# Kernel tuning notes

Measured on AMD Instinct MI355X. Metric: run time of the kernel, lower is better.

## Reference

```python
import jax, jax.numpy as jnp
import numpy as np

OUT_FEATURES = 4096
IN_FEATURES = 4096
GROUP_SIZE = 128


def setup_inputs() -> dict:
    key = jax.random.key(0)
    k1, k2, k3, k4, k5 = jax.random.split(key, 5)
    x = jax.random.normal(k1, (4, 2048, IN_FEATURES), dtype=jnp.float32)
    # two 4-bit codes per byte-like int32 element
    packed = jax.random.randint(k2, (OUT_FEATURES * IN_FEATURES // 2,), 0, 256, dtype=jnp.int32)
    n_groups = OUT_FEATURES * IN_FEATURES // GROUP_SIZE
    scales = jax.random.uniform(k3, (n_groups,), dtype=jnp.float32) * 0.02 + 1e-3
    offsets = jax.random.normal(k4, (n_groups,), dtype=jnp.float32) * 0.01
    bias = jax.random.normal(k5, (OUT_FEATURES,), dtype=jnp.float32)
    return {"x": x, "packed": packed, "scales": scales, "offsets": offsets, "bias": bias}


def _dequant(packed, scales, offsets):
    # unpack low/high nibbles -> int codes in [0, 15]
    low = packed & 0xF
    high = (packed >> 4) & 0xF
    codes = jnp.stack([low, high], axis=-1).reshape(-1).astype(jnp.float32)  # [out*in]
    # per-group affine dequant: w = code * scale + offset
    w = codes.reshape(-1, GROUP_SIZE) * scales[:, None] + offsets[:, None]
    return w.reshape(OUT_FEATURES, IN_FEATURES)


def reference(x, packed, scales, offsets, bias):
    weight = _dequant(packed, scales, offsets)  # [out, in]
    # F.linear: x @ W^T + b
    return jnp.einsum('bsi,oi->bso', x, weight) + bias
```

## Files before the change

kernel.cpp:

```cpp
#include <hip/hip_runtime.h>
#include <hip/hip_bf16.h>
#include <stdint.h>

#define IN_F   4096
#define OUT_F  4096
#define M_TOT  8192

typedef __bf16 bf16x8 __attribute__((ext_vector_type(8)));
typedef float  floatx4 __attribute__((ext_vector_type(4)));

__device__ __forceinline__ unsigned f2bf_bits(float f) {
    union { float f; uint32_t u; } v; v.f = f;
    uint32_t r = v.u + 0x7FFF + ((v.u >> 16) & 1);
    return r >> 16;
}

__device__ __forceinline__ void gl_lds16(const void* g, void* l) {
    __builtin_amdgcn_global_load_lds(
        (const __attribute__((address_space(1))) void*)g,
        (__attribute__((address_space(3))) void*)l, 16, 0, 0);
}

#define X_BLOCKS 16384
#define W_BLOCKS 8192

__global__ void prep_kernel(const float* __restrict__ x, ushort* __restrict__ xb,
                            const int* __restrict__ packed,
                            const float* __restrict__ scales,
                            const float* __restrict__ offsets,
                            ushort* __restrict__ wb) {
    if (blockIdx.x < X_BLOCKS) {
        int i = blockIdx.x * 256 + threadIdx.x;
        float4 v0 = reinterpret_cast<const float4*>(x)[2 * i];
        float4 v1 = reinterpret_cast<const float4*>(x)[2 * i + 1];
        uint4 o;
        o.x = f2bf_bits(v0.x) | (f2bf_bits(v0.y) << 16);
        o.y = f2bf_bits(v0.z) | (f2bf_bits(v0.w) << 16);
        o.z = f2bf_bits(v1.x) | (f2bf_bits(v1.y) << 16);
        o.w = f2bf_bits(v1.z) | (f2bf_bits(v1.w) << 16);
        reinterpret_cast<uint4*>(xb)[i] = o;
    } else {
        int i = (blockIdx.x - X_BLOCKS) * 256 + threadIdx.x;
        int4 p = reinterpret_cast<const int4*>(packed)[i];
        int g = i >> 4;
        float s = scales[g], off = offsets[g];
        uint4 ov;
        ov.x = f2bf_bits((float)(p.x & 0xF) * s + off) |
               (f2bf_bits((float)((p.x >> 4) & 0xF) * s + off) << 16);
        ov.y = f2bf_bits((float)(p.y & 0xF) * s + off) |
               (f2bf_bits((float)((p.y >> 4) & 0xF) * s + off) << 16);
        ov.z = f2bf_bits((float)(p.z & 0xF) * s + off) |
               (f2bf_bits((float)((p.z >> 4) & 0xF) * s + off) << 16);
        ov.w = f2bf_bits((float)(p.w & 0xF) * s + off) |
               (f2bf_bits((float)((p.w >> 4) & 0xF) * s + off) << 16);
        reinterpret_cast<uint4*>(wb)[i] = ov;
    }
}

__global__ void gemm_kernel(const ushort* __restrict__ A,
                            const ushort* __restrict__ B,
                            const float* __restrict__ bias,
                            float* __restrict__ C) {
    __shared__ __align__(16) ushort As[128 * 32];
    __shared__ __align__(16) ushort Bs[128 * 32];

    const int tid  = threadIdx.x;
    const int wave = tid >> 6;
    const int lane = tid & 63;
    const int quad = lane >> 4;
    const int l16  = lane & 15;
    const int wm   = wave >> 1;
    const int wn   = wave & 1;

    const int bm = blockIdx.y;
    const int bn = blockIdx.x;

    const int c0 = tid, c1 = 256 + tid;
    const int r0 = c0 >> 2, l0 = (c0 & 3) ^ ((r0 >> 1) & 3);
    const int r1 = c1 >> 2, l1 = (c1 & 3) ^ ((r1 >> 1) & 3);

    const ushort* gA0 = A + (size_t)(bm * 128 + r0) * IN_F + l0 * 8;
    const ushort* gA1 = A + (size_t)(bm * 128 + r1) * IN_F + l1 * 8;
    const ushort* gB0 = B + (size_t)(bn * 128 + r0) * IN_F + l0 * 8;
    const ushort* gB1 = B + (size_t)(bn * 128 + r1) * IN_F + l1 * 8;

    char* lA0 = (char*)As + wave * 1024;
    char* lA1 = (char*)As + 4096 + wave * 1024;
    char* lB0 = (char*)Bs + wave * 1024;
    char* lB1 = (char*)Bs + 4096 + wave * 1024;

    floatx4 acc[4][4] = {};

    const int arow = wm * 64 + l16;
    const int brow = wn * 64 + l16;
    const int koff = (quad ^ ((l16 >> 1) & 3)) * 8;

    for (int k0 = 0; k0 < IN_F; k0 += 32) {
        gl_lds16(gA0, lA0);
        gl_lds16(gA1, lA1);
        gl_lds16(gB0, lB0);
        gl_lds16(gB1, lB1);
        gA0 += 32; gA1 += 32; gB0 += 32; gB1 += 32;
        __syncthreads();

        bf16x8 af[4], bfr[4];
#pragma unroll
        for (int mi = 0; mi < 4; ++mi)
            af[mi] = *reinterpret_cast<const bf16x8*>(&As[(arow + mi * 16) * 32 + koff]);
#pragma unroll
        for (int ni = 0; ni < 4; ++ni)
            bfr[ni] = *reinterpret_cast<const bf16x8*>(&Bs[(brow + ni * 16) * 32 + koff]);

#pragma unroll
        for (int mi = 0; mi < 4; ++mi)
#pragma unroll
            for (int ni = 0; ni < 4; ++ni)
                acc[mi][ni] = __builtin_amdgcn_mfma_f32_16x16x32_bf16(
                    af[mi], bfr[ni], acc[mi][ni], 0, 0, 0);

        __syncthreads();
    }

    const float* biasp = bias + bn * 128 + wn * 64 + l16;
    float* Cp = C + (size_t)(bm * 128 + wm * 64 + quad * 4) * OUT_F + bn * 128 + wn * 64 + l16;
#pragma unroll
    for (int mi = 0; mi < 4; ++mi) {
#pragma unroll
        for (int ni = 0; ni < 4; ++ni) {
            float bv = biasp[ni * 16];
#pragma unroll
            for (int r = 0; r < 4; ++r)
                Cp[(size_t)(mi * 16 + r) * OUT_F + ni * 16] = acc[mi][ni][r] + bv;
        }
    }
}

extern "C" void kernel_launch(void* const* d_in, const int* in_sizes, int n_in,
                              void* d_out, int out_size, void* d_ws, size_t ws_size,
                              hipStream_t stream) {
    const float* x       = (const float*)d_in[0];
    const int*   packed  = (const int*)d_in[1];
    const float* scales  = (const float*)d_in[2];
    const float* offsets = (const float*)d_in[3];
    const float* bias    = (const float*)d_in[4];
    float* out = (float*)d_out;

    ushort* xb = (ushort*)d_ws;
    ushort* wb = (ushort*)((char*)d_ws + (size_t)M_TOT * IN_F * 2);

    prep_kernel<<<X_BLOCKS + W_BLOCKS, 256, 0, stream>>>(x, xb, packed, scales, offsets, wb);

    dim3 grid(OUT_F / 128, M_TOT / 128);
    gemm_kernel<<<grid, 256, 0, stream>>>(xb, wb, bias, out);
}
```

Before: 549.4 us.

## Fuse fp32-to-bf16 activation conversion into GEMM tile loads

Drops the separate pass that converted the activations to bf16 in workspace. The GEMM now streams fp32 activation tiles straight into LDS with a new XOR swizzle and converts them to bf16 in registers before the MFMA. This removes a full read and write of the activation tensor, but doubles the A-tile global traffic and LDS footprint per k-step and repeats the conversion once for each of the 32 column blocks.

```diff
diff --git a/kernel.cpp b/kernel.cpp
--- a/kernel.cpp
+++ b/kernel.cpp
@@ -21,47 +21,31 @@
         (__attribute__((address_space(3))) void*)l, 16, 0, 0);
 }
 
-#define X_BLOCKS 16384
-#define W_BLOCKS 8192
-
-__global__ void prep_kernel(const float* __restrict__ x, ushort* __restrict__ xb,
-                            const int* __restrict__ packed,
-                            const float* __restrict__ scales,
-                            const float* __restrict__ offsets,
-                            ushort* __restrict__ wb) {
-    if (blockIdx.x < X_BLOCKS) {
-        int i = blockIdx.x * 256 + threadIdx.x;
-        float4 v0 = reinterpret_cast<const float4*>(x)[2 * i];
-        float4 v1 = reinterpret_cast<const float4*>(x)[2 * i + 1];
-        uint4 o;
-        o.x = f2bf_bits(v0.x) | (f2bf_bits(v0.y) << 16);
-        o.y = f2bf_bits(v0.z) | (f2bf_bits(v0.w) << 16);
-        o.z = f2bf_bits(v1.x) | (f2bf_bits(v1.y) << 16);
-        o.w = f2bf_bits(v1.z) | (f2bf_bits(v1.w) << 16);
-        reinterpret_cast<uint4*>(xb)[i] = o;
-    } else {
-        int i = (blockIdx.x - X_BLOCKS) * 256 + threadIdx.x;
-        int4 p = reinterpret_cast<const int4*>(packed)[i];
-        int g = i >> 4;
-        float s = scales[g], off = offsets[g];
-        uint4 ov;
-        ov.x = f2bf_bits((float)(p.x & 0xF) * s + off) |
-               (f2bf_bits((float)((p.x >> 4) & 0xF) * s + off) << 16);
-        ov.y = f2bf_bits((float)(p.y & 0xF) * s + off) |
-               (f2bf_bits((float)((p.y >> 4) & 0xF) * s + off) << 16);
-        ov.z = f2bf_bits((float)(p.z & 0xF) * s + off) |
-               (f2bf_bits((float)((p.z >> 4) & 0xF) * s + off) << 16);
-        ov.w = f2bf_bits((float)(p.w & 0xF) * s + off) |
-               (f2bf_bits((float)((p.w >> 4) & 0xF) * s + off) << 16);
-        reinterpret_cast<uint4*>(wb)[i] = ov;
-    }
+__global__ void dequant_kernel(const int* __restrict__ packed,
+                               const float* __restrict__ scales,
+                               const float* __restrict__ offsets,
+                               ushort* __restrict__ wb) {
+    int i = blockIdx.x * 256 + threadIdx.x;
+    int4 p = reinterpret_cast<const int4*>(packed)[i];
+    int g = i >> 4;
+    float s = scales[g], off = offsets[g];
+    uint4 ov;
+    ov.x = f2bf_bits((float)(p.x & 0xF) * s + off) |
+           (f2bf_bits((float)((p.x >> 4) & 0xF) * s + off) << 16);
+    ov.y = f2bf_bits((float)(p.y & 0xF) * s + off) |
+           (f2bf_bits((float)((p.y >> 4) & 0xF) * s + off) << 16);
+    ov.z = f2bf_bits((float)(p.z & 0xF) * s + off) |
+           (f2bf_bits((float)((p.z >> 4) & 0xF) * s + off) << 16);
+    ov.w = f2bf_bits((float)(p.w & 0xF) * s + off) |
+           (f2bf_bits((float)((p.w >> 4) & 0xF) * s + off) << 16);
+    reinterpret_cast<uint4*>(wb)[i] = ov;
 }
 
-__global__ void gemm_kernel(const ushort* __restrict__ A,
+__global__ void gemm_kernel(const float* __restrict__ A,
                             const ushort* __restrict__ B,
                             const float* __restrict__ bias,
                             float* __restrict__ C) {
-    __shared__ __align__(16) ushort As[128 * 32];
+    __shared__ __align__(16) float  Asf[128 * 32];
     __shared__ __align__(16) ushort Bs[128 * 32];
 
     const int tid  = threadIdx.x;
@@ -75,38 +59,55 @@
     const int bm = blockIdx.y;
     const int bn = blockIdx.x;
 
-    const int c0 = tid, c1 = 256 + tid;
-    const int r0 = c0 >> 2, l0 = (c0 & 3) ^ ((r0 >> 1) & 3);
-    const int r1 = c1 >> 2, l1 = (c1 & 3) ^ ((r1 >> 1) & 3);
+    const int ar = tid >> 3;
+    const int al = (tid & 7) ^ (ar & 7);
+    const float* gA0 = A + (size_t)(bm * 128 +  0 + ar) * IN_F + al * 4;
+    const float* gA1 = A + (size_t)(bm * 128 + 32 + ar) * IN_F + al * 4;
+    const float* gA2 = A + (size_t)(bm * 128 + 64 + ar) * IN_F + al * 4;
+    const float* gA3 = A + (size_t)(bm * 128 + 96 + ar) * IN_F + al * 4;
 
-    const ushort* gA0 = A + (size_t)(bm * 128 + r0) * IN_F + l0 * 8;
-    const ushort* gA1 = A + (size_t)(bm * 128 + r1) * IN_F + l1 * 8;
-    const ushort* gB0 = B + (size_t)(bn * 128 + r0) * IN_F + l0 * 8;
-    const ushort* gB1 = B + (size_t)(bn * 128 + r1) * IN_F + l1 * 8;
+    const int br = tid >> 2;
+    const int bl = (tid & 3) ^ ((tid >> 3) & 3);
+    const ushort* gB0 = B + (size_t)(bn * 128 +  0 + br) * IN_F + bl * 8;
+    const ushort* gB1 = B + (size_t)(bn * 128 + 64 + br) * IN_F + bl * 8;
 
-    char* lA0 = (char*)As + wave * 1024;
-    char* lA1 = (char*)As + 4096 + wave * 1024;
-    char* lB0 = (char*)Bs + wave * 1024;
-    char* lB1 = (char*)Bs + 4096 + wave * 1024;
+    char* lA0 = (char*)Asf + 0 * 4096 + wave * 1024;
+    char* lA1 = (char*)Asf + 1 * 4096 + wave * 1024;
+    char* lA2 = (char*)Asf + 2 * 4096 + wave * 1024;
+    char* lA3 = (char*)Asf + 3 * 4096 + wave * 1024;
+    char* lB0 = (char*)Bs + 0 * 4096 + wave * 1024;
+    char* lB1 = (char*)Bs + 1 * 4096 + wave * 1024;
 
     floatx4 acc[4][4] = {};
 
     const int arow = wm * 64 + l16;
     const int brow = wn * 64 + l16;
+    const int aswz = l16 & 7;
+    const int ac0  = ((2 * quad)     ^ aswz) * 4;
+    const int ac1  = ((2 * quad + 1) ^ aswz) * 4;
     const int koff = (quad ^ ((l16 >> 1) & 3)) * 8;
 
     for (int k0 = 0; k0 < IN_F; k0 += 32) {
-        gl_lds16(gA0, lA0);
-        gl_lds16(gA1, lA1);
-        gl_lds16(gB0, lB0);
-        gl_lds16(gB1, lB1);
-        gA0 += 32; gA1 += 32; gB0 += 32; gB1 += 32;
+        gl_lds16(gA0, lA0); gl_lds16(gA1, lA1);
+        gl_lds16(gA2, lA2); gl_lds16(gA3, lA3);
+        gl_lds16(gB0, lB0); gl_lds16(gB1, lB1);
+        gA0 += 32; gA1 += 32; gA2 += 32; gA3 += 32;
+        gB0 += 32; gB1 += 32;
         __syncthreads();
 
         bf16x8 af[4], bfr[4];
 #pragma unroll
-        for (int mi = 0; mi < 4; ++mi)
-            af[mi] = *reinterpret_cast<const bf16x8*>(&As[(arow + mi * 16) * 32 + koff]);
+        for (int mi = 0; mi < 4; ++mi) {
+            const float* rowp = &Asf[(arow + mi * 16) * 32];
+            float4 f0 = *reinterpret_cast<const float4*>(rowp + ac0);
+            float4 f1 = *reinterpret_cast<const float4*>(rowp + ac1);
+            bf16x8 v;
+            v[0] = (__bf16)f0.x; v[1] = (__bf16)f0.y;
+            v[2] = (__bf16)f0.z; v[3] = (__bf16)f0.w;
+            v[4] = (__bf16)f1.x; v[5] = (__bf16)f1.y;
+            v[6] = (__bf16)f1.z; v[7] = (__bf16)f1.w;
+            af[mi] = v;
+        }
 #pragma unroll
         for (int ni = 0; ni < 4; ++ni)
             bfr[ni] = *reinterpret_cast<const bf16x8*>(&Bs[(brow + ni * 16) * 32 + koff]);
@@ -145,11 +146,10 @@
     const float* bias    = (const float*)d_in[4];
     float* out = (float*)d_out;
 
-    ushort* xb = (ushort*)d_ws;
-    ushort* wb = (ushort*)((char*)d_ws + (size_t)M_TOT * IN_F * 2);
+    ushort* wb = (ushort*)d_ws;
 
-    prep_kernel<<<X_BLOCKS + W_BLOCKS, 256, 0, stream>>>(x, xb, packed, scales, offsets, wb);
+    dequant_kernel<<<8192, 256, 0, stream>>>(packed, scales, offsets, wb);
 
     dim3 grid(OUT_F / 128, M_TOT / 128);
-    gemm_kernel<<<grid, 256, 0, stream>>>(xb, wb, bias, out);
+    gemm_kernel<<<grid, 256, 0, stream>>>(x, wb, bias, out);
 }
```

New measurement: 632.1 us. 1.15x slower.
